# Kernel tuning notes

Hardware: AMD Instinct MI355X
Metric: run time of the kernel (lower is better)

The kernel has to match this reference:

```python
import jax, jax.numpy as jnp
import numpy as np
from jax import lax

B, C_IN, C_OUT, K, W_DIM, H, W = 16, 512, 512, 3, 512, 64, 64


def setup_inputs() -> dict:
    key = jax.random.key(0)
    k1, k2, k3, k4, k5 = jax.random.split(key, 5)
    fan_in = C_IN * K * K
    bound = 1.0 / np.sqrt(fan_in)
    imgs = jax.random.normal(k1, (B, C_IN, H, W), dtype=jnp.float32)
    w_embs = jax.random.normal(k2, (B, W_DIM), dtype=jnp.float32)
    conv_weight = jax.random.uniform(k3, (C_OUT, C_IN, K, K), jnp.float32, -bound, bound)
    conv_bias = jax.random.uniform(k4, (C_OUT,), jnp.float32, -bound, bound)
    sb = 1.0 / np.sqrt(W_DIM)
    style_W = jax.random.uniform(k5, (C_IN, W_DIM), jnp.float32, -sb, sb)
    style_b = jnp.zeros((C_IN,), jnp.float32)
    return {"imgs": imgs, "w_embs": w_embs, "conv_weight": conv_weight,
            "conv_bias": conv_bias, "style_W": style_W, "style_b": style_b}


def reference(imgs, w_embs, conv_weight, conv_bias, style_W, style_b):
    b, c, h, w = imgs.shape
    out_dim, in_dim, ky, kx = conv_weight.shape
    # style modulation: (b, in_dim), +1 as in the torch module
    style = w_embs @ style_W.T + style_b + 1.0
    # per-sample weights: (b, out_dim, in_dim, ky, kx)
    weight = conv_weight[None] * style[:, None, :, None, None]
    # demodulation: exact L2 norm over (in_dim, ky, kx) (no eps, matching torch)
    norm = jnp.sqrt(jnp.sum(weight * weight, axis=(2, 3, 4), keepdims=True))
    weight = weight / norm
    # grouped conv with groups = batch
    x = imgs.reshape(1, b * c, h, w)
    k = weight.reshape(b * out_dim, in_dim, ky, kx)
    y = lax.conv_general_dilated(
        x, k, window_strides=(1, 1), padding="SAME",
        feature_group_count=b,
        dimension_numbers=("NCHW", "OIHW", "NCHW"))
    y = y.reshape(b, out_dim, h, w)
    return y + conv_bias[None, :, None, None]
```

## Files before the change

### kernel.cpp

```cpp
#include <hip/hip_runtime.h>


typedef __bf16 bf16x8 __attribute__((ext_vector_type(8)));
typedef float f32x4 __attribute__((ext_vector_type(4)));

__device__ __forceinline__ void async16(const void* g, void* s) {
  __builtin_amdgcn_global_load_lds((const __attribute__((address_space(1))) void*)g,
                                   (__attribute__((address_space(3))) void*)s, 16, 0, 0);
}

__global__ __launch_bounds__(256) void k_style(const float* __restrict__ we,
                                               const float* __restrict__ sW,
                                               const float* __restrict__ sb,
                                               float* __restrict__ style) {
  int lane = threadIdx.x & 63, wid = threadIdx.x >> 6;
  int b = blockIdx.x >> 7;
  int i = ((blockIdx.x & 127) << 2) + wid;
  const float* wer = we + b * 512;
  const float* swr = sW + i * 512;
  float acc = 0.f;
  for (int d = lane; d < 512; d += 64) acc += wer[d] * swr[d];
#pragma unroll
  for (int off = 32; off; off >>= 1) acc += __shfl_xor(acc, off);
  if (lane == 0) style[b * 512 + i] = acc + sb[i] + 1.0f;
}

__global__ __launch_bounds__(256) void k_wsq(const float* __restrict__ cw,
                                             float* __restrict__ wsq) {
  int t = blockIdx.x * 256 + threadIdx.x;
  const float* p = cw + (long)t * 9;
  float s = 0.f;
#pragma unroll
  for (int k = 0; k < 9; ++k) s += p[k] * p[k];
  wsq[t] = s;
}

__global__ __launch_bounds__(256) void k_rnorm(const float* __restrict__ style,
                                               const float* __restrict__ wsq,
                                               float* __restrict__ rnorm) {
  int lane = threadIdx.x & 63, wid = threadIdx.x >> 6;
  int idx = blockIdx.x * 4 + wid;
  int b = idx >> 9, o = idx & 511;
  float acc = 0.f;
  for (int i = lane; i < 512; i += 64) {
    float s = style[(b << 9) + i];
    acc += s * s * wsq[(o << 9) + i];
  }
#pragma unroll
  for (int off = 32; off; off >>= 1) acc += __shfl_xor(acc, off);
  if (lane == 0) rnorm[idx] = rsqrtf(acc);
}

__global__ __launch_bounds__(256) void k_wt(const float* __restrict__ cw,
                                            const float* __restrict__ style,
                                            const float* __restrict__ rnorm,
                                            __bf16* __restrict__ wt) {
  int t = blockIdx.x * 256 + threadIdx.x;
  int b = t >> 18;
  int oi = t & 262143;
  int o = oi >> 9, i = oi & 511;
  float sc = style[(b << 9) + i] * rnorm[(b << 9) + o];
  const float* p = cw + (long)oi * 9;
#pragma unroll
  for (int k = 0; k < 9; ++k)
    wt[((long)(b * 9 + k) << 18) + ((long)o << 9) + i] = (__bf16)(p[k] * sc);
}

__global__ __launch_bounds__(256) void k_xpad(const float* __restrict__ imgs,
                                              __bf16* __restrict__ xpad) {
  int t = blockIdx.x * 256 + threadIdx.x;
  if (t >= 16 * 4356) return;
  int b = t / 4356;
  int rc = t - b * 4356;
  int r = rc / 66, c = rc - (rc / 66) * 66;
  __bf16* dst = xpad + (long)t * 512;
  if (r == 0 || r == 65 || c == 0 || c == 65) {
    const f32x4 z = {0.f, 0.f, 0.f, 0.f};
#pragma unroll 4
    for (int j = 0; j < 64; ++j) *(f32x4*)(dst + j * 8) = z;
  } else {
    const float* src = imgs + ((long)b << 21) + ((r - 1) << 6) + (c - 1);
    for (int j = 0; j < 64; ++j) {
      bf16x8 v;
#pragma unroll
      for (int q = 0; q < 8; ++q) v[q] = (__bf16)src[(long)(j * 8 + q) << 12];
      *(bf16x8*)(dst + j * 8) = v;
    }
  }
}

__global__ __launch_bounds__(256, 3) void k_conv(const __bf16* __restrict__ xpad,
                                                 const __bf16* __restrict__ wt,
                                                 const float* __restrict__ bias,
                                                 float* __restrict__ out) {
  __shared__ __attribute__((aligned(16))) __bf16 sX[224 * 64];
  __shared__ __attribute__((aligned(16))) __bf16 sA[128 * 64];

  const int tid = threadIdx.x;
  const int lane = tid & 63;
  const int wid = tid >> 6;
  const int wr = wid >> 1, wc = wid & 1;
  const int l15 = lane & 15, lq = lane >> 4, l7 = lane & 7;

  const int bid = blockIdx.x;
  const int b = bid >> 7;
  const int r7 = bid & 127;
  const int o0 = (r7 >> 5) << 7;
  const int st = r7 & 31;
  const int h0 = (st >> 1) << 2;
  const int w0 = (st & 1) << 5;

  const __bf16* xg[7];
#pragma unroll
  for (int it = 0; it < 7; ++it) {
    int s = it * 256 + tid;
    int p = s >> 3;
    int pp = (p < 204) ? p : 0;
    int j = (s & 7) ^ (pp & 7);
    int lr = pp / 34, lc = pp - lr * 34;
    xg[it] = xpad + ((long)((b * 66 + h0 + lr) * 66) + (w0 + lc)) * 512 + j * 8;
  }
  int aoff[4];
#pragma unroll
  for (int it = 0; it < 4; ++it) {
    int s = it * 256 + tid;
    int row = s >> 3;
    int j = (s & 7) ^ (row & 7);
    aoff[it] = ((o0 + row) << 9) + (j << 3);
  }
  const __bf16* wtb = wt + (long)b * (9 * 512 * 512);

  f32x4 acc[4][4];
  const f32x4 zero4 = {0.f, 0.f, 0.f, 0.f};
#pragma unroll
  for (int m = 0; m < 4; ++m)
#pragma unroll
    for (int n = 0; n < 4; ++n) acc[m][n] = zero4;

  int prn[4], pcn[4];
#pragma unroll
  for (int n = 0; n < 4; ++n) {
    int nn = (wc << 6) + (n << 4) + l15;
    prn[n] = nn >> 5;
    pcn[n] = nn & 31;
  }
  const int arow = ((wr << 6) + l15) << 6;

  for (int ic = 0; ic < 512; ic += 64) {
#pragma unroll
    for (int t = 0; t < 9; ++t) {
      __syncthreads();
      if (t == 0) {
#pragma unroll
        for (int it = 0; it < 7; ++it)
          async16(xg[it] + ic, (char*)sX + (it * 256 + (wid << 6)) * 16);
      }
      {
        const __bf16* wa = wtb + t * (512 * 512) + ic;
#pragma unroll
        for (int it = 0; it < 4; ++it)
          async16(wa + aoff[it], (char*)sA + (it * 256 + (wid << 6)) * 16);
      }
      __syncthreads();
      const int ky = t / 3, kx = t - (t / 3) * 3;
#pragma unroll
      for (int kk = 0; kk < 2; ++kk) {
        const int jb = lq + (kk << 2);
        const int jA = (jb ^ l7) << 3;
        bf16x8 af[4], bf[4];
#pragma unroll
        for (int m = 0; m < 4; ++m)
          af[m] = *(const bf16x8*)&sA[arow + (m << 10) + jA];
#pragma unroll
        for (int n = 0; n < 4; ++n) {
          int p = (prn[n] + ky) * 34 + pcn[n] + kx;
          bf[n] = *(const bf16x8*)&sX[(p << 6) + ((jb ^ (p & 7)) << 3)];
        }
#pragma unroll
        for (int m = 0; m < 4; ++m)
#pragma unroll
          for (int n = 0; n < 4; ++n)
            acc[m][n] = __builtin_amdgcn_mfma_f32_16x16x32_bf16(af[m], bf[n],
                                                                acc[m][n], 0, 0, 0);
      }
    }
  }

  float* outb = out + ((long)b << 21);
#pragma unroll
  for (int m = 0; m < 4; ++m) {
    int ob = o0 + (wr << 6) + (m << 4) + (lq << 2);
#pragma unroll
    for (int n = 0; n < 4; ++n) {
      int h = h0 + prn[n], w = w0 + pcn[n];
#pragma unroll
      for (int q = 0; q < 4; ++q) {
        int o = ob + q;
        outb[((long)o << 12) + (h << 6) + w] = acc[m][n][q] + bias[o];
      }
    }
  }
}

extern "C" void kernel_launch(void* const* d_in, const int* in_sizes, int n_in,
                              void* d_out, int out_size, void* d_ws, size_t ws_size,
                              hipStream_t stream) {
  const float* imgs = (const float*)d_in[0];
  const float* w_embs = (const float*)d_in[1];
  const float* cw = (const float*)d_in[2];
  const float* bias = (const float*)d_in[3];
  const float* style_W = (const float*)d_in[4];
  const float* style_b = (const float*)d_in[5];
  float* out = (float*)d_out;

  char* ws = (char*)d_ws;
  float* style = (float*)(ws);
  float* rnorm = (float*)(ws + (32 << 10));
  float* wsq = (float*)(ws + (64 << 10));
  __bf16* wt = (__bf16*)(ws + (64 << 10) + (1 << 20));
  __bf16* xpad = (__bf16*)(ws + (64 << 10) + (1 << 20) + 75497472);
  size_t need = (size_t)(64 << 10) + (1 << 20) + 75497472ull + 71368704ull;
  if (ws_size < need) return;

  k_style<<<2048, 256, 0, stream>>>(w_embs, style_W, style_b, style);
  k_wsq<<<1024, 256, 0, stream>>>(cw, wsq);
  k_rnorm<<<2048, 256, 0, stream>>>(style, wsq, rnorm);
  k_wt<<<16384, 256, 0, stream>>>(cw, style, rnorm, wt);
  k_xpad<<<273, 256, 0, stream>>>(imgs, xpad);
  k_conv<<<2048, 256, 0, stream>>>(xpad, wt, bias, out);
}
```

Before: 393.9 us.

## Double-buffer weight tiles and enlarge conv tile to 128x256 outputs

The conv kernel now computes a 128-channel by 256-pixel tile per block (8 output rows instead of 4), doubling the per-wave accumulator count and halving the grid. Weight tiles are double-buffered in LDS, so the next tap's weights are prefetched asynchronously while MFMAs run on the current buffer, with explicit vmcnt waits and raw barriers in place of __syncthreads. It also sets wave priority around the MFMA section. The aim is better operand reuse and hiding global-to-LDS latency, at the cost of more registers and LDS and occupancy dropping to 2 blocks per CU.

Measured after the change: 629.2 us. 1.6x slower.

```diff
diff --git a/kernel.cpp b/kernel.cpp
--- a/kernel.cpp
+++ b/kernel.cpp
@@ -89,110 +89,139 @@
   }
 }
 
-__global__ __launch_bounds__(256, 3) void k_conv(const __bf16* __restrict__ xpad,
+__global__ __launch_bounds__(256, 2) void k_conv(const __bf16* __restrict__ xpad,
                                                  const __bf16* __restrict__ wt,
                                                  const float* __restrict__ bias,
                                                  float* __restrict__ out) {
-  __shared__ __attribute__((aligned(16))) __bf16 sX[224 * 64];
-  __shared__ __attribute__((aligned(16))) __bf16 sA[128 * 64];
+  __shared__ __attribute__((aligned(16))) __bf16 sAe[2 * 8192];
+  __shared__ __attribute__((aligned(16))) __bf16 sX[22528];
 
   const int tid = threadIdx.x;
   const int lane = tid & 63;
   const int wid = tid >> 6;
-  const int wr = wid >> 1, wc = wid & 1;
+  const int wo = wid >> 1, wp = wid & 1;
   const int l15 = lane & 15, lq = lane >> 4, l7 = lane & 7;
 
   const int bid = blockIdx.x;
-  const int b = bid >> 7;
-  const int r7 = bid & 127;
-  const int o0 = (r7 >> 5) << 7;
-  const int st = r7 & 31;
-  const int h0 = (st >> 1) << 2;
+  const int b = bid >> 6;
+  const int r6 = bid & 63;
+  const int o0 = (r6 >> 4) << 7;
+  const int st = r6 & 15;
+  const int h0 = (st >> 1) << 3;
   const int w0 = (st & 1) << 5;
-
-  const __bf16* xg[7];
-#pragma unroll
-  for (int it = 0; it < 7; ++it) {
+  const int b66 = b * 66;
+
+  const __bf16* xg[11];
+#pragma unroll
+  for (int it = 0; it < 11; ++it) {
     int s = it * 256 + tid;
+    if (s > 2719) s = 2719;
     int p = s >> 3;
-    int pp = (p < 204) ? p : 0;
-    int j = (s & 7) ^ (pp & 7);
-    int lr = pp / 34, lc = pp - lr * 34;
-    xg[it] = xpad + ((long)((b * 66 + h0 + lr) * 66) + (w0 + lc)) * 512 + j * 8;
-  }
-  int aoff[4];
-#pragma unroll
-  for (int it = 0; it < 4; ++it) {
-    int s = it * 256 + tid;
-    int row = s >> 3;
-    int j = (s & 7) ^ (row & 7);
-    aoff[it] = ((o0 + row) << 9) + (j << 3);
-  }
-  const __bf16* wtb = wt + (long)b * (9 * 512 * 512);
-
-  f32x4 acc[4][4];
+    int j = (s & 7) ^ (p & 7);
+    int lr = p / 34, lc = p - (p / 34) * 34;
+    xg[it] = xpad + ((long)((b66 + h0 + lr) * 66) + (w0 + lc)) * 512 + j * 8;
+  }
+  int aoff0;
+  {
+    int row = tid >> 3;
+    int j = (tid & 7) ^ (row & 7);
+    aoff0 = ((o0 + row) << 9) + (j << 3);
+  }
+  const __bf16* wtb = wt + (long)b * 2359296;
+
+  f32x4 acc[4][8];
   const f32x4 zero4 = {0.f, 0.f, 0.f, 0.f};
 #pragma unroll
   for (int m = 0; m < 4; ++m)
 #pragma unroll
-    for (int n = 0; n < 4; ++n) acc[m][n] = zero4;
-
-  int prn[4], pcn[4];
+    for (int n = 0; n < 8; ++n) acc[m][n] = zero4;
+
+  int pbase[4];
 #pragma unroll
   for (int n = 0; n < 4; ++n) {
-    int nn = (wc << 6) + (n << 4) + l15;
-    prn[n] = nn >> 5;
-    pcn[n] = nn & 31;
-  }
-  const int arow = ((wr << 6) + l15) << 6;
-
-  for (int ic = 0; ic < 512; ic += 64) {
+    int nn = (wp << 7) + (n << 4) + l15;
+    pbase[n] = (nn >> 5) * 34 + (nn & 31);
+  }
+  const int arowb = ((wo << 6) + l15) << 6;
+
+#pragma unroll
+  for (int it = 0; it < 11; ++it)
+    async16(xg[it], (char*)sX + it * 4096 + (wid << 10));
+#pragma unroll
+  for (int it = 0; it < 4; ++it)
+    async16(wtb + aoff0 + it * 16384, (char*)sAe + it * 4096 + (wid << 10));
+  asm volatile("s_waitcnt vmcnt(0)" ::: "memory");
+  __builtin_amdgcn_sched_barrier(0);
+  __builtin_amdgcn_s_barrier();
+
+  for (int icb = 0; icb < 8; ++icb) {
+    const int ic = icb << 6;
 #pragma unroll
     for (int t = 0; t < 9; ++t) {
-      __syncthreads();
-      if (t == 0) {
-#pragma unroll
-        for (int it = 0; it < 7; ++it)
-          async16(xg[it] + ic, (char*)sX + (it * 256 + (wid << 6)) * 16);
-      }
-      {
-        const __bf16* wa = wtb + t * (512 * 512) + ic;
-#pragma unroll
-        for (int it = 0; it < 4; ++it)
-          async16(wa + aoff[it], (char*)sA + (it * 256 + (wid << 6)) * 16);
-      }
-      __syncthreads();
+      const int cur = (icb + t) & 1;
+      if (t == 0 && icb > 0) {
+#pragma unroll
+        for (int it = 0; it < 11; ++it)
+          async16(xg[it] + ic, (char*)sX + it * 4096 + (wid << 10));
+      }
+      if (!(icb == 7 && t == 8)) {
+        const int tn = (t == 8) ? 0 : t + 1;
+        const int icn = ic + ((t == 8) ? 64 : 0);
+        const __bf16* wa = wtb + tn * 262144 + icn + aoff0;
+        char* dst = (char*)sAe + (cur ^ 1) * 16384 + (wid << 10);
+#pragma unroll
+        for (int it = 0; it < 4; ++it) async16(wa + it * 16384, dst + it * 4096);
+      }
+      if (icb == 7 && t == 8) {
+        asm volatile("s_waitcnt vmcnt(0)" ::: "memory");
+      } else {
+        asm volatile("s_waitcnt vmcnt(4)" ::: "memory");
+      }
+      __builtin_amdgcn_sched_barrier(0);
+      __builtin_amdgcn_s_barrier();
+      __builtin_amdgcn_sched_barrier(0);
       const int ky = t / 3, kx = t - (t / 3) * 3;
+      const int kshift = ky * 34 + kx;
+      const __bf16* sAb = sAe + cur * 8192;
+      __builtin_amdgcn_s_setprio(1);
 #pragma unroll
       for (int kk = 0; kk < 2; ++kk) {
         const int jb = lq + (kk << 2);
         const int jA = (jb ^ l7) << 3;
-        bf16x8 af[4], bf[4];
+        bf16x8 af[4];
 #pragma unroll
         for (int m = 0; m < 4; ++m)
-          af[m] = *(const bf16x8*)&sA[arow + (m << 10) + jA];
-#pragma unroll
-        for (int n = 0; n < 4; ++n) {
-          int p = (prn[n] + ky) * 34 + pcn[n] + kx;
-          bf[n] = *(const bf16x8*)&sX[(p << 6) + ((jb ^ (p & 7)) << 3)];
+          af[m] = *(const bf16x8*)&sAb[arowb + (m << 10) + jA];
+#pragma unroll
+        for (int nh = 0; nh < 2; ++nh) {
+          bf16x8 bfr[4];
+#pragma unroll
+          for (int n2 = 0; n2 < 4; ++n2) {
+            int p = pbase[n2] + nh * 68 + kshift;
+            bfr[n2] = *(const bf16x8*)&sX[(p << 6) + ((jb ^ (p & 7)) << 3)];
+          }
+#pragma unroll
+          for (int m = 0; m < 4; ++m)
+#pragma unroll
+            for (int n2 = 0; n2 < 4; ++n2)
+              acc[m][(nh << 2) + n2] = __builtin_amdgcn_mfma_f32_16x16x32_bf16(
+                  af[m], bfr[n2], acc[m][(nh << 2) + n2], 0, 0, 0);
         }
-#pragma unroll
-        for (int m = 0; m < 4; ++m)
-#pragma unroll
-          for (int n = 0; n < 4; ++n)
-            acc[m][n] = __builtin_amdgcn_mfma_f32_16x16x32_bf16(af[m], bf[n],
-                                                                acc[m][n], 0, 0, 0);
-      }
+      }
+      __builtin_amdgcn_s_setprio(0);
+      __builtin_amdgcn_sched_barrier(0);
+      __builtin_amdgcn_s_barrier();
     }
   }
 
   float* outb = out + ((long)b << 21);
 #pragma unroll
   for (int m = 0; m < 4; ++m) {
-    int ob = o0 + (wr << 6) + (m << 4) + (lq << 2);
-#pragma unroll
-    for (int n = 0; n < 4; ++n) {
-      int h = h0 + prn[n], w = w0 + pcn[n];
+    int ob = o0 + (wo << 6) + (m << 4) + (lq << 2);
+#pragma unroll
+    for (int n = 0; n < 8; ++n) {
+      int pid = (wp << 7) + (n << 4) + l15;
+      int h = h0 + (pid >> 5), w = w0 + (pid & 31);
 #pragma unroll
       for (int q = 0; q < 4; ++q) {
         int o = ob + q;
@@ -227,5 +256,5 @@
   k_rnorm<<<2048, 256, 0, stream>>>(style, wsq, rnorm);
   k_wt<<<16384, 256, 0, stream>>>(cw, style, rnorm, wt);
   k_xpad<<<273, 256, 0, stream>>>(imgs, xpad);
-  k_conv<<<2048, 256, 0, stream>>>(xpad, wt, bias, out);
-}
+  k_conv<<<1024, 256, 0, stream>>>(xpad, wt, bias, out);
+}
```

## Double-buffer weight tiles in conv kernel to prefetch the next tap

Applied to the files above, without the earlier changes.

The per-tap weight tile in LDS is now double-buffered. The next tap's (or next channel block's) weights are loaded asynchronously while the current tap's MFMAs run, synchronised with explicit vmcnt waits and raw s_barrier instead of two __syncthreads per tap. Wave priority is raised around the MFMA section, and the occupancy hint drops from 3 to 2 blocks per CU to make room for the extra LDS. The input tile reload at each channel-block boundary is still not overlapped with compute.

New measurement: 427.8 us. 8.6% more time.

```diff
diff --git a/kernel.cpp b/kernel.cpp
--- a/kernel.cpp
+++ b/kernel.cpp
@@ -89,12 +89,12 @@
   }
 }
 
-__global__ __launch_bounds__(256, 3) void k_conv(const __bf16* __restrict__ xpad,
+__global__ __launch_bounds__(256, 2) void k_conv(const __bf16* __restrict__ xpad,
                                                  const __bf16* __restrict__ wt,
                                                  const float* __restrict__ bias,
                                                  float* __restrict__ out) {
   __shared__ __attribute__((aligned(16))) __bf16 sX[224 * 64];
-  __shared__ __attribute__((aligned(16))) __bf16 sA[128 * 64];
+  __shared__ __attribute__((aligned(16))) __bf16 sAe[2 * 8192];
 
   const int tid = threadIdx.x;
   const int lane = tid & 63;
@@ -120,15 +120,13 @@
     int lr = pp / 34, lc = pp - lr * 34;
     xg[it] = xpad + ((long)((b * 66 + h0 + lr) * 66) + (w0 + lc)) * 512 + j * 8;
   }
-  int aoff[4];
-#pragma unroll
-  for (int it = 0; it < 4; ++it) {
-    int s = it * 256 + tid;
-    int row = s >> 3;
-    int j = (s & 7) ^ (row & 7);
-    aoff[it] = ((o0 + row) << 9) + (j << 3);
-  }
-  const __bf16* wtb = wt + (long)b * (9 * 512 * 512);
+  int aoff0;
+  {
+    int row = tid >> 3;
+    int j = (tid & 7) ^ (row & 7);
+    aoff0 = ((o0 + row) << 9) + (j << 3);
+  }
+  const __bf16* wtb = wt + (long)b * 2359296;
 
   f32x4 acc[4][4];
   const f32x4 zero4 = {0.f, 0.f, 0.f, 0.f};
@@ -144,45 +142,70 @@
     prn[n] = nn >> 5;
     pcn[n] = nn & 31;
   }
-  const int arow = ((wr << 6) + l15) << 6;
-
-  for (int ic = 0; ic < 512; ic += 64) {
+  const int arowb = ((wr << 6) + l15) << 6;
+
+#pragma unroll
+  for (int it = 0; it < 7; ++it)
+    async16(xg[it], (char*)sX + it * 4096 + (wid << 10));
+#pragma unroll
+  for (int it = 0; it < 4; ++it)
+    async16(wtb + aoff0 + it * 16384, (char*)sAe + it * 4096 + (wid << 10));
+  asm volatile("s_waitcnt vmcnt(0)" ::: "memory");
+  __builtin_amdgcn_sched_barrier(0);
+  __builtin_amdgcn_s_barrier();
+
+  for (int icb = 0; icb < 8; ++icb) {
+    const int ic = icb << 6;
 #pragma unroll
     for (int t = 0; t < 9; ++t) {
-      __syncthreads();
-      if (t == 0) {
+      const int cur = (icb + t) & 1;
+      if (t == 0 && icb > 0) {
 #pragma unroll
         for (int it = 0; it < 7; ++it)
-          async16(xg[it] + ic, (char*)sX + (it * 256 + (wid << 6)) * 16);
-      }
-      {
-        const __bf16* wa = wtb + t * (512 * 512) + ic;
-#pragma unroll
-        for (int it = 0; it < 4; ++it)
-          async16(wa + aoff[it], (char*)sA + (it * 256 + (wid << 6)) * 16);
-      }
-      __syncthreads();
+          async16(xg[it] + ic, (char*)sX + it * 4096 + (wid << 10));
+      }
+      if (!(icb == 7 && t == 8)) {
+        const int tn = (t == 8) ? 0 : t + 1;
+        const int icn = ic + ((t == 8) ? 64 : 0);
+        const __bf16* wa = wtb + tn * 262144 + icn + aoff0;
+        char* dst = (char*)sAe + (cur ^ 1) * 16384 + (wid << 10);
+#pragma unroll
+        for (int it = 0; it < 4; ++it) async16(wa + it * 16384, dst + it * 4096);
+      }
+      if (icb == 7 && t == 8) {
+        asm volatile("s_waitcnt vmcnt(0)" ::: "memory");
+      } else {
+        asm volatile("s_waitcnt vmcnt(4)" ::: "memory");
+      }
+      __builtin_amdgcn_sched_barrier(0);
+      __builtin_amdgcn_s_barrier();
+      __builtin_amdgcn_sched_barrier(0);
       const int ky = t / 3, kx = t - (t / 3) * 3;
+      const __bf16* sAb = sAe + cur * 8192;
+      __builtin_amdgcn_s_setprio(1);
 #pragma unroll
       for (int kk = 0; kk < 2; ++kk) {
         const int jb = lq + (kk << 2);
         const int jA = (jb ^ l7) << 3;
-        bf16x8 af[4], bf[4];
+        bf16x8 af[4], bfr[4];
 #pragma unroll
         for (int m = 0; m < 4; ++m)
-          af[m] = *(const bf16x8*)&sA[arow + (m << 10) + jA];
+          af[m] = *(const bf16x8*)&sAb[arowb + (m << 10) + jA];
 #pragma unroll
         for (int n = 0; n < 4; ++n) {
           int p = (prn[n] + ky) * 34 + pcn[n] + kx;
-          bf[n] = *(const bf16x8*)&sX[(p << 6) + ((jb ^ (p & 7)) << 3)];
+          bfr[n] = *(const bf16x8*)&sX[(p << 6) + ((jb ^ (p & 7)) << 3)];
         }
 #pragma unroll
         for (int m = 0; m < 4; ++m)
 #pragma unroll
           for (int n = 0; n < 4; ++n)
-            acc[m][n] = __builtin_amdgcn_mfma_f32_16x16x32_bf16(af[m], bf[n],
+            acc[m][n] = __builtin_amdgcn_mfma_f32_16x16x32_bf16(af[m], bfr[n],
                                                                 acc[m][n], 0, 0, 0);
       }
+      __builtin_amdgcn_s_setprio(0);
+      __builtin_amdgcn_sched_barrier(0);
+      __builtin_amdgcn_s_barrier();
     }
   }
 
```

## Pre-pack weights in MFMA fragment order and load A directly from global

Applied to the files above, without the earlier changes.

The weight-prep kernel now writes per-sample weights in the exact MFMA A-fragment layout (per tap, input-channel block, 16-row output tile and k-half), so each lane can load its fragment with one contiguous 16-byte global load. The conv kernel drops the shared-memory A tile and its two barriers per tap, and syncs only once per 64-channel block to refill the input tile. This removes LDS traffic and synchronisation for weights. The cost is fragment loads that go straight to global/L2 memory with no staging, which may expose latency, and a less coalesced weight-prep kernel.

Result: slower. 929.4 us (+135.9%).

```diff
diff --git a/kernel.cpp b/kernel.cpp
--- a/kernel.cpp
+++ b/kernel.cpp
@@ -54,16 +54,26 @@
 __global__ __launch_bounds__(256) void k_wt(const float* __restrict__ cw,
                                             const float* __restrict__ style,
                                             const float* __restrict__ rnorm,
-                                            __bf16* __restrict__ wt) {
-  int t = blockIdx.x * 256 + threadIdx.x;
-  int b = t >> 18;
-  int oi = t & 262143;
-  int o = oi >> 9, i = oi & 511;
-  float sc = style[(b << 9) + i] * rnorm[(b << 9) + o];
-  const float* p = cw + (long)oi * 9;
-#pragma unroll
-  for (int k = 0; k < 9; ++k)
-    wt[((long)(b * 9 + k) << 18) + ((long)o << 9) + i] = (__bf16)(p[k] * sc);
+                                            __bf16* __restrict__ wt2) {
+  int tid = blockIdx.x * 256 + threadIdx.x;
+  int lane = tid & 63;
+  int kk = (tid >> 6) & 1;
+  int ot = (tid >> 7) & 31;
+  int icb = (tid >> 12) & 7;
+  int bt = tid >> 15;
+  int b = bt / 9, t = bt - 9 * b;
+  int o = (ot << 4) + (lane & 15);
+  int ic0 = (icb << 6) + (kk << 5) + ((lane >> 4) << 3);
+  float rn = rnorm[(b << 9) + o];
+  const float* cwo = cw + ((long)o << 9) * 9 + t;
+  const float* stb = style + (b << 9);
+  bf16x8 v;
+#pragma unroll
+  for (int j = 0; j < 8; ++j) {
+    int ic = ic0 + j;
+    v[j] = (__bf16)(cwo[(long)ic * 9] * stb[ic] * rn);
+  }
+  *(bf16x8*)(wt2 + (long)tid * 8) = v;
 }
 
 __global__ __launch_bounds__(256) void k_xpad(const float* __restrict__ imgs,
@@ -90,17 +100,16 @@
 }
 
 __global__ __launch_bounds__(256, 3) void k_conv(const __bf16* __restrict__ xpad,
-                                                 const __bf16* __restrict__ wt,
+                                                 const __bf16* __restrict__ wt2,
                                                  const float* __restrict__ bias,
                                                  float* __restrict__ out) {
   __shared__ __attribute__((aligned(16))) __bf16 sX[224 * 64];
-  __shared__ __attribute__((aligned(16))) __bf16 sA[128 * 64];
 
   const int tid = threadIdx.x;
   const int lane = tid & 63;
   const int wid = tid >> 6;
   const int wr = wid >> 1, wc = wid & 1;
-  const int l15 = lane & 15, lq = lane >> 4, l7 = lane & 7;
+  const int l15 = lane & 15, lq = lane >> 4;
 
   const int bid = blockIdx.x;
   const int b = bid >> 7;
@@ -120,15 +129,7 @@
     int lr = pp / 34, lc = pp - lr * 34;
     xg[it] = xpad + ((long)((b * 66 + h0 + lr) * 66) + (w0 + lc)) * 512 + j * 8;
   }
-  int aoff[4];
-#pragma unroll
-  for (int it = 0; it < 4; ++it) {
-    int s = it * 256 + tid;
-    int row = s >> 3;
-    int j = (s & 7) ^ (row & 7);
-    aoff[it] = ((o0 + row) << 9) + (j << 3);
-  }
-  const __bf16* wtb = wt + (long)b * (9 * 512 * 512);
+  const int otb = (o0 >> 4) + (wr << 2);
 
   f32x4 acc[4][4];
   const f32x4 zero4 = {0.f, 0.f, 0.f, 0.f};
@@ -144,45 +145,45 @@
     prn[n] = nn >> 5;
     pcn[n] = nn & 31;
   }
-  const int arow = ((wr << 6) + l15) << 6;
-
-  for (int ic = 0; ic < 512; ic += 64) {
+
+#pragma unroll
+  for (int it = 0; it < 7; ++it)
+    async16(xg[it], (char*)sX + it * 4096 + (wid << 10));
+
+  for (int icb = 0; icb < 8; ++icb) {
+    __syncthreads();
 #pragma unroll
     for (int t = 0; t < 9; ++t) {
-      __syncthreads();
-      if (t == 0) {
-#pragma unroll
-        for (int it = 0; it < 7; ++it)
-          async16(xg[it] + ic, (char*)sX + (it * 256 + (wid << 6)) * 16);
-      }
-      {
-        const __bf16* wa = wtb + t * (512 * 512) + ic;
-#pragma unroll
-        for (int it = 0; it < 4; ++it)
-          async16(wa + aoff[it], (char*)sA + (it * 256 + (wid << 6)) * 16);
-      }
-      __syncthreads();
       const int ky = t / 3, kx = t - (t / 3) * 3;
+      const __bf16* ab =
+          wt2 + ((((long)(b * 9 + t) * 8 + icb) * 32 + otb) * 2) * 512 +
+          (lane << 3);
 #pragma unroll
       for (int kk = 0; kk < 2; ++kk) {
         const int jb = lq + (kk << 2);
-        const int jA = (jb ^ l7) << 3;
-        bf16x8 af[4], bf[4];
+        bf16x8 af[4], bfr[4];
 #pragma unroll
         for (int m = 0; m < 4; ++m)
-          af[m] = *(const bf16x8*)&sA[arow + (m << 10) + jA];
+          af[m] = *(const bf16x8*)(ab + (((m << 1) + kk) << 9));
 #pragma unroll
         for (int n = 0; n < 4; ++n) {
           int p = (prn[n] + ky) * 34 + pcn[n] + kx;
-          bf[n] = *(const bf16x8*)&sX[(p << 6) + ((jb ^ (p & 7)) << 3)];
+          bfr[n] = *(const bf16x8*)&sX[(p << 6) + ((jb ^ (p & 7)) << 3)];
         }
 #pragma unroll
         for (int m = 0; m < 4; ++m)
 #pragma unroll
           for (int n = 0; n < 4; ++n)
-            acc[m][n] = __builtin_amdgcn_mfma_f32_16x16x32_bf16(af[m], bf[n],
+            acc[m][n] = __builtin_amdgcn_mfma_f32_16x16x32_bf16(af[m], bfr[n],
                                                                 acc[m][n], 0, 0, 0);
       }
+    }
+    if (icb < 7) {
+      __syncthreads();
+      const int icn = (icb + 1) << 6;
+#pragma unroll
+      for (int it = 0; it < 7; ++it)
+        async16(xg[it] + icn, (char*)sX + it * 4096 + (wid << 10));
     }
   }
 
@@ -217,7 +218,7 @@
   float* style = (float*)(ws);
   float* rnorm = (float*)(ws + (32 << 10));
   float* wsq = (float*)(ws + (64 << 10));
-  __bf16* wt = (__bf16*)(ws + (64 << 10) + (1 << 20));
+  __bf16* wt2 = (__bf16*)(ws + (64 << 10) + (1 << 20));
   __bf16* xpad = (__bf16*)(ws + (64 << 10) + (1 << 20) + 75497472);
   size_t need = (size_t)(64 << 10) + (1 << 20) + 75497472ull + 71368704ull;
   if (ws_size < need) return;
@@ -225,7 +226,7 @@
   k_style<<<2048, 256, 0, stream>>>(w_embs, style_W, style_b, style);
   k_wsq<<<1024, 256, 0, stream>>>(cw, wsq);
   k_rnorm<<<2048, 256, 0, stream>>>(style, wsq, rnorm);
-  k_wt<<<16384, 256, 0, stream>>>(cw, style, rnorm, wt);
+  k_wt<<<18432, 256, 0, stream>>>(cw, style, rnorm, wt2);
   k_xpad<<<273, 256, 0, stream>>>(imgs, xpad);
-  k_conv<<<2048, 256, 0, stream>>>(xpad, wt, bias, out);
-}
+  k_conv<<<2048, 256, 0, stream>>>(xpad, wt2, bias, out);
+}
```
